# Optimization experiments

Measured on AMD Instinct MI355X. Metric: run time of the kernel, lower is better.

## Reference

```python
import jax, jax.numpy as jnp
import numpy as np
from jax.scipy.special import logsumexp

TEMPERATURE = 0.05
HARD_NEG_WEIGHT = 1.0
MARGIN = 0.2
EXPLICIT_NEG_WEIGHT = 2.0
NEG_INF = -1e9


def setup_inputs() -> dict:
    key = jax.random.key(0)
    k1, k2, k3 = jax.random.split(key, 3)
    N, D = 8192, 512
    return {
        "asm_embeddings": jax.random.normal(k1, (N, D), dtype=jnp.float32),
        "source_embeddings": jax.random.normal(k2, (N, D), dtype=jnp.float32),
        "labels": jax.random.randint(k3, (N,), 0, 2, dtype=jnp.int64),
    }


def reference(asm_embeddings, source_embeddings, labels):
    # L2-normalize both embedding sets
    a = asm_embeddings / jnp.linalg.norm(asm_embeddings, axis=1, keepdims=True)
    s = source_embeddings / jnp.linalg.norm(source_embeddings, axis=1, keepdims=True)
    sim = jnp.matmul(a, s.T) / TEMPERATURE  # [N, N]

    N = labels.shape[0]
    pos_mask = labels == 1
    neg_mask = labels == 0
    num_pos = jnp.sum(pos_mask).astype(sim.dtype)
    num_neg = jnp.sum(neg_mask)

    # column weights: explicit negatives (label==0) get EXPLICIT_NEG_WEIGHT,
    # others 1; the positive (diagonal) logit always has weight 1.
    log_w = jnp.log(jnp.where(neg_mask, EXPLICIT_NEG_WEIGHT, 1.0).astype(sim.dtype))
    eye = jnp.eye(N, dtype=bool)
    weighted_logits = sim + jnp.where(eye, 0.0, log_w[None, :])  # [N, N]

    lse = logsumexp(weighted_logits, axis=1)  # weighted logsumexp per row
    diag = jnp.diagonal(sim)
    per_row_loss = lse - diag  # -log_prob_pos

    infonce = jnp.sum(jnp.where(pos_mask, per_row_loss, 0.0)) / num_pos

    # margin penalty on hardest explicit-negative diagonal similarity
    mean_pos_sim = jnp.sum(jnp.where(pos_mask, diag, 0.0)) / num_pos
    hard_neg_sim = jnp.max(jnp.where(neg_mask, diag, NEG_INF))
    penalty = jax.nn.relu(hard_neg_sim - mean_pos_sim + MARGIN)
    penalty = jnp.where(num_neg > 0, penalty, 0.0)

    return infonce + HARD_NEG_WEIGHT * penalty
```

## Files before the change

kernel.cpp:

```cpp
#include <hip/hip_runtime.h>
#include <math.h>

#define NROWS 8192
#define DIM 512
#define INV_T 20.0f
#define QS 500.0f
#define DEQ2 (INV_T * 1.4426950408889634f / (QS * QS))

typedef __attribute__((ext_vector_type(4))) int i32x4;

__device__ __forceinline__ void gload_lds16(const void* g, void* l) {
    __builtin_amdgcn_global_load_lds(
        (const __attribute__((address_space(1))) unsigned int*)g,
        (__attribute__((address_space(3))) unsigned int*)l, 16, 0, 0);
}

__device__ __forceinline__ float hw_exp2(float x) {
    float r;
    asm("v_exp_f32 %0, %1" : "=v"(r) : "v"(x));
    return r;
}

__device__ __forceinline__ float dot4(float4 a, float4 b) {
    return a.x * b.x + a.y * b.y + a.z * b.z + a.w * b.w;
}

__device__ __forceinline__ int q4(float4 v, float s) {
    int b0 = __float2int_rn(fminf(fmaxf(v.x * s, -127.f), 127.f)) & 255;
    int b1 = __float2int_rn(fminf(fmaxf(v.y * s, -127.f), 127.f)) & 255;
    int b2 = __float2int_rn(fminf(fmaxf(v.z * s, -127.f), 127.f)) & 255;
    int b3 = __float2int_rn(fminf(fmaxf(v.w * s, -127.f), 127.f)) & 255;
    return b0 | (b1 << 8) | (b2 << 16) | (b3 << 24);
}

__global__ __launch_bounds__(256) void norm_kernel(
    const float* __restrict__ A, const float* __restrict__ S,
    const int* __restrict__ labels, signed char* __restrict__ aQ,
    signed char* __restrict__ sQ, float* __restrict__ diag,
    float* __restrict__ lw2, float* __restrict__ lsum) {
    const int wave = threadIdx.x >> 6, lane = threadIdx.x & 63;
    const int row = blockIdx.x * 4 + wave;
    const float4* a4 = (const float4*)(A + (size_t)row * DIM);
    const float4* s4 = (const float4*)(S + (size_t)row * DIM);
    float4 a0 = a4[lane], a1 = a4[lane + 64];
    float4 s0 = s4[lane], s1 = s4[lane + 64];
    float saa = dot4(a0, a0) + dot4(a1, a1);
    float sss = dot4(s0, s0) + dot4(s1, s1);
    float sas = dot4(a0, s0) + dot4(a1, s1);
    for (int m = 1; m < 64; m <<= 1) {
        saa += __shfl_xor(saa, m);
        sss += __shfl_xor(sss, m);
        sas += __shfl_xor(sas, m);
    }
    const float ra = rsqrtf(saa), rs = rsqrtf(sss);
    signed char* arow = aQ + (size_t)row * DIM;
    signed char* srow = sQ + (size_t)row * DIM;
    *(int*)(arow + lane * 4)       = q4(a0, ra * QS);
    *(int*)(arow + 256 + lane * 4) = q4(a1, ra * QS);
    *(int*)(srow + lane * 4)       = q4(s0, rs * QS);
    *(int*)(srow + 256 + lane * 4) = q4(s1, rs * QS);
    if (lane == 0) {
        diag[row] = sas * ra * rs * INV_T;
        lw2[row] = (labels[row] == 0) ? 1.0f : 0.0f;
        lsum[row] = 0.0f;
    }
}

__global__ __launch_bounds__(1024) void lse_gemm(
    const signed char* __restrict__ Aq, const signed char* __restrict__ Bq,
    const float* __restrict__ lw2, float* __restrict__ lsum) {
    __shared__ __align__(16) char lds[65536];

    const int bid = blockIdx.x;
    const int xcd = bid & 7, idx = bid >> 3;
    const int rt = (xcd >> 1) * 8 + (idx & 7);
    const int ctg = (xcd & 1) * 4 + (idx >> 3);
    const int row0 = rt * 256;
    const int colg = ctg * 1024;

    const int tid = threadIdx.x;
    const int wid = tid >> 6, lane = tid & 63;
    const int wr = wid >> 2, wc = wid & 3;
    const int fr = lane & 15, grp = lane >> 4;

    const int srow = tid >> 2;
    const int sl = (tid & 3) ^ ((tid >> 3) & 3);
    const signed char* aSrc = Aq + (size_t)(row0 + srow) * DIM + sl * 16;
    const signed char* bSrc = Bq + (size_t)(colg + srow) * DIM + sl * 16;
    char* dstA = lds + tid * 16;
    char* dstB = lds + 16384 + tid * 16;

#define STAGE(buf, TT)                                                        \
    do {                                                                      \
        const int ct_ = (TT) >> 3, k_ = (TT) & 7;                             \
        gload_lds16(aSrc + k_ * 64, dstA + (buf) * 32768);                    \
        gload_lds16(bSrc + ct_ * 131072 + k_ * 64, dstB + (buf) * 32768);     \
    } while (0)

    const int ps = (grp ^ ((fr >> 1) & 3)) << 4;
    const char* rdA = lds + (wr * 64 + fr) * 64 + ps;
    const char* rdB = lds + 16384 + (wc * 64 + fr) * 64 + ps;

    STAGE(0, 0);

    i32x4 acc[4][4] = {};
#pragma unroll 2
    for (int T = 0; T < 32; ++T) {
        const int buf = T & 1;
        if (T < 31) {
            STAGE(buf ^ 1, T + 1);
            asm volatile("s_waitcnt vmcnt(2)" ::: "memory");
        } else {
            asm volatile("s_waitcnt vmcnt(0)" ::: "memory");
        }
        __builtin_amdgcn_s_barrier();

        i32x4 a[4], b[4];
#pragma unroll
        for (int m = 0; m < 4; ++m)
            a[m] = *(const i32x4*)(rdA + buf * 32768 + m * 1024);
#pragma unroll
        for (int n = 0; n < 4; ++n)
            b[n] = *(const i32x4*)(rdB + buf * 32768 + n * 1024);
        asm volatile("s_waitcnt lgkmcnt(0)" ::: "memory");
        __builtin_amdgcn_sched_barrier(0);

        __builtin_amdgcn_s_setprio(1);
#pragma unroll
        for (int m = 0; m < 4; ++m)
#pragma unroll
            for (int n = 0; n < 4; ++n)
                acc[m][n] = __builtin_amdgcn_mfma_i32_16x16x64_i8(
                    a[m], b[n], acc[m][n], 0, 0, 0);
        __builtin_amdgcn_s_setprio(0);

        if ((T & 7) == 7) {
            const int ct = T >> 3;
            const int col0 = colg + ct * 256 + wc * 64;
            float lwv[4];
#pragma unroll
            for (int n = 0; n < 4; ++n)
                lwv[n] = lw2[col0 + n * 16 + fr];
#pragma unroll
            for (int m = 0; m < 4; ++m)
#pragma unroll
                for (int j = 0; j < 4; ++j) {
                    float s = 0.f;
#pragma unroll
                    for (int n = 0; n < 4; ++n)
                        s += hw_exp2(fmaf((float)acc[m][n][j], DEQ2, lwv[n]));
                    s += __shfl_xor(s, 1);
                    s += __shfl_xor(s, 2);
                    s += __shfl_xor(s, 4);
                    s += __shfl_xor(s, 8);
                    if (fr == 0)
                        atomicAdd(&lsum[row0 + wr * 64 + m * 16 + grp * 4 + j], s);
                }
#pragma unroll
            for (int m = 0; m < 4; ++m)
#pragma unroll
                for (int n = 0; n < 4; ++n)
                    acc[m][n] = i32x4{0, 0, 0, 0};
        }
        __builtin_amdgcn_s_barrier();
    }
#undef STAGE
}

__global__ __launch_bounds__(1024) void finalize_kernel(
    const float* __restrict__ lsum, const float* __restrict__ diag,
    const int* __restrict__ labels, float* __restrict__ out) {
    const int tid = threadIdx.x;
    float sl = 0.f, sd = 0.f, mx = -1e9f;
    int np_ = 0, nn_ = 0;
#pragma unroll
    for (int i = tid; i < NROWS; i += 1024) {
        const float dg = diag[i];
        if (labels[i] == 1) {
            sl += logf(lsum[i]) - dg;
            sd += dg;
            np_++;
        } else {
            nn_++;
            mx = fmaxf(mx, dg);
        }
    }
    for (int m = 1; m < 64; m <<= 1) {
        sl += __shfl_xor(sl, m);
        sd += __shfl_xor(sd, m);
        mx = fmaxf(mx, __shfl_xor(mx, m));
        np_ += __shfl_xor(np_, m);
        nn_ += __shfl_xor(nn_, m);
    }
    __shared__ float rsl[16], rsd[16], rmx[16];
    __shared__ int rnp[16], rnn[16];
    const int wave = tid >> 6, lane = tid & 63;
    if (lane == 0) {
        rsl[wave] = sl; rsd[wave] = sd; rmx[wave] = mx;
        rnp[wave] = np_; rnn[wave] = nn_;
    }
    __syncthreads();
    if (tid == 0) {
        float SL = 0.f, SD = 0.f, MX = -1e9f;
        int NP = 0, NN = 0;
        for (int w = 0; w < 16; w++) {
            SL += rsl[w]; SD += rsd[w]; MX = fmaxf(MX, rmx[w]);
            NP += rnp[w]; NN += rnn[w];
        }
        const float infonce = SL / (float)NP;
        const float meanpos = SD / (float)NP;
        float pen = fmaxf(MX - meanpos + 0.2f, 0.0f);
        if (NN == 0) pen = 0.0f;
        out[0] = infonce + pen;
    }
}

extern "C" void kernel_launch(void* const* d_in, const int* in_sizes, int n_in,
                              void* d_out, int out_size, void* d_ws, size_t ws_size,
                              hipStream_t stream) {
    const float* A = (const float*)d_in[0];
    const float* S = (const float*)d_in[1];
    const int* labels = (const int*)d_in[2];
    float* out = (float*)d_out;

    char* ws = (char*)d_ws;
    signed char* aQ = (signed char*)ws;
    signed char* sQ = (signed char*)(ws + (size_t)NROWS * DIM);
    char* p = ws + (size_t)NROWS * DIM * 2;
    float* diag = (float*)p;
    float* lw2 = (float*)(p + 32768);
    float* lsum = (float*)(p + 65536);

    norm_kernel<<<NROWS / 4, 256, 0, stream>>>(A, S, labels, aQ, sQ, diag, lw2, lsum);
    lse_gemm<<<256, 1024, 0, stream>>>(aQ, sQ, lw2, lsum);
    finalize_kernel<<<1, 1024, 0, stream>>>(lsum, diag, labels, out);
}
```

Baseline: 65.77 us.

## Retile LSE GEMM to 512-thread blocks with register-accumulated row sums

The int8 similarity GEMM now uses 512-thread blocks with 8 waves in a 4x2 layout. Each block covers 256 rows by 512 columns, processed as four 128-column tiles, and 512 blocks are launched. LDS per block drops to 48KB, which should allow more resident blocks per CU. Row exp-sums are now kept in registers across the column tiles, with one shuffle-and-atomic reduction at the end instead of one per tile. In exchange, each wave now loads A twice per stage and the total A-tile traffic doubles, and B tiles are reused across fewer rows per column.

```diff
diff --git a/kernel.cpp b/kernel.cpp
--- a/kernel.cpp
+++ b/kernel.cpp
@@ -66,35 +66,35 @@
     }
 }
 
-__global__ __launch_bounds__(1024) void lse_gemm(
+__global__ __launch_bounds__(512, 4) void lse_gemm(
     const signed char* __restrict__ Aq, const signed char* __restrict__ Bq,
     const float* __restrict__ lw2, float* __restrict__ lsum) {
-    __shared__ __align__(16) char lds[65536];
+    __shared__ __align__(16) char lds[49152];
 
     const int bid = blockIdx.x;
     const int xcd = bid & 7, idx = bid >> 3;
     const int rt = (xcd >> 1) * 8 + (idx & 7);
-    const int ctg = (xcd & 1) * 4 + (idx >> 3);
+    const int ctg = (xcd & 1) * 8 + (idx >> 3);
     const int row0 = rt * 256;
-    const int colg = ctg * 1024;
+    const int colg = ctg * 512;
 
     const int tid = threadIdx.x;
     const int wid = tid >> 6, lane = tid & 63;
-    const int wr = wid >> 2, wc = wid & 3;
+    const int wr = wid >> 1, wc = wid & 1;
     const int fr = lane & 15, grp = lane >> 4;
 
-    const int srow = tid >> 2;
     const int sl = (tid & 3) ^ ((tid >> 3) & 3);
-    const signed char* aSrc = Aq + (size_t)(row0 + srow) * DIM + sl * 16;
-    const signed char* bSrc = Bq + (size_t)(colg + srow) * DIM + sl * 16;
+    const signed char* aSrc = Aq + (size_t)(row0 + (tid >> 2)) * DIM + sl * 16;
+    const signed char* bSrc = Bq + (size_t)(colg + (tid >> 2)) * DIM + sl * 16;
     char* dstA = lds + tid * 16;
     char* dstB = lds + 16384 + tid * 16;
 
 #define STAGE(buf, TT)                                                        \
     do {                                                                      \
         const int ct_ = (TT) >> 3, k_ = (TT) & 7;                             \
-        gload_lds16(aSrc + k_ * 64, dstA + (buf) * 32768);                    \
-        gload_lds16(bSrc + ct_ * 131072 + k_ * 64, dstB + (buf) * 32768);     \
+        gload_lds16(aSrc + k_ * 64,           dstA + (buf) * 24576);          \
+        gload_lds16(aSrc + 65536 + k_ * 64,   dstA + (buf) * 24576 + 8192);   \
+        gload_lds16(bSrc + ct_ * 65536 + k_ * 64, dstB + (buf) * 24576);      \
     } while (0)
 
     const int ps = (grp ^ ((fr >> 1) & 3)) << 4;
@@ -103,68 +103,78 @@
 
     STAGE(0, 0);
 
+    float rsum[4][4] = {};
     i32x4 acc[4][4] = {};
-#pragma unroll 2
-    for (int T = 0; T < 32; ++T) {
-        const int buf = T & 1;
-        if (T < 31) {
-            STAGE(buf ^ 1, T + 1);
-            asm volatile("s_waitcnt vmcnt(2)" ::: "memory");
-        } else {
-            asm volatile("s_waitcnt vmcnt(0)" ::: "memory");
-        }
-        __builtin_amdgcn_s_barrier();
-
-        i32x4 a[4], b[4];
+
+#pragma unroll
+    for (int ct = 0; ct < 4; ++ct) {
+#pragma unroll
+        for (int k = 0; k < 8; ++k) {
+            const int T = ct * 8 + k;
+            const int buf = T & 1;
+            if (T < 31) {
+                STAGE(buf ^ 1, T + 1);
+                asm volatile("s_waitcnt vmcnt(3)" ::: "memory");
+            } else {
+                asm volatile("s_waitcnt vmcnt(0)" ::: "memory");
+            }
+            __builtin_amdgcn_s_barrier();
+
+            i32x4 a[4], b[4];
+#pragma unroll
+            for (int m = 0; m < 4; ++m)
+                a[m] = *(const i32x4*)(rdA + buf * 24576 + m * 1024);
+#pragma unroll
+            for (int n = 0; n < 4; ++n)
+                b[n] = *(const i32x4*)(rdB + buf * 24576 + n * 1024);
+            asm volatile("s_waitcnt lgkmcnt(0)" ::: "memory");
+            __builtin_amdgcn_sched_barrier(0);
+
+            __builtin_amdgcn_s_setprio(1);
+#pragma unroll
+            for (int m = 0; m < 4; ++m)
+#pragma unroll
+                for (int n = 0; n < 4; ++n)
+                    acc[m][n] = __builtin_amdgcn_mfma_i32_16x16x64_i8(
+                        a[m], b[n], acc[m][n], 0, 0, 0);
+            __builtin_amdgcn_s_setprio(0);
+            __builtin_amdgcn_s_barrier();
+        }
+
+        const int col0 = colg + ct * 128 + wc * 64;
+        float lwv[4];
+#pragma unroll
+        for (int n = 0; n < 4; ++n)
+            lwv[n] = lw2[col0 + n * 16 + fr];
 #pragma unroll
         for (int m = 0; m < 4; ++m)
-            a[m] = *(const i32x4*)(rdA + buf * 32768 + m * 1024);
-#pragma unroll
-        for (int n = 0; n < 4; ++n)
-            b[n] = *(const i32x4*)(rdB + buf * 32768 + n * 1024);
-        asm volatile("s_waitcnt lgkmcnt(0)" ::: "memory");
-        __builtin_amdgcn_sched_barrier(0);
-
-        __builtin_amdgcn_s_setprio(1);
+#pragma unroll
+            for (int j = 0; j < 4; ++j) {
+#pragma unroll
+                for (int n = 0; n < 4; ++n)
+                    rsum[m][j] +=
+                        hw_exp2(fmaf((float)acc[m][n][j], DEQ2, lwv[n]));
+            }
 #pragma unroll
         for (int m = 0; m < 4; ++m)
 #pragma unroll
             for (int n = 0; n < 4; ++n)
-                acc[m][n] = __builtin_amdgcn_mfma_i32_16x16x64_i8(
-                    a[m], b[n], acc[m][n], 0, 0, 0);
-        __builtin_amdgcn_s_setprio(0);
-
-        if ((T & 7) == 7) {
-            const int ct = T >> 3;
-            const int col0 = colg + ct * 256 + wc * 64;
-            float lwv[4];
-#pragma unroll
-            for (int n = 0; n < 4; ++n)
-                lwv[n] = lw2[col0 + n * 16 + fr];
-#pragma unroll
-            for (int m = 0; m < 4; ++m)
-#pragma unroll
-                for (int j = 0; j < 4; ++j) {
-                    float s = 0.f;
-#pragma unroll
-                    for (int n = 0; n < 4; ++n)
-                        s += hw_exp2(fmaf((float)acc[m][n][j], DEQ2, lwv[n]));
-                    s += __shfl_xor(s, 1);
-                    s += __shfl_xor(s, 2);
-                    s += __shfl_xor(s, 4);
-                    s += __shfl_xor(s, 8);
-                    if (fr == 0)
-                        atomicAdd(&lsum[row0 + wr * 64 + m * 16 + grp * 4 + j], s);
-                }
-#pragma unroll
-            for (int m = 0; m < 4; ++m)
-#pragma unroll
-                for (int n = 0; n < 4; ++n)
-                    acc[m][n] = i32x4{0, 0, 0, 0};
-        }
-        __builtin_amdgcn_s_barrier();
+                acc[m][n] = i32x4{0, 0, 0, 0};
     }
 #undef STAGE
+
+#pragma unroll
+    for (int m = 0; m < 4; ++m)
+#pragma unroll
+        for (int j = 0; j < 4; ++j) {
+            float v = rsum[m][j];
+            v += __shfl_xor(v, 1);
+            v += __shfl_xor(v, 2);
+            v += __shfl_xor(v, 4);
+            v += __shfl_xor(v, 8);
+            if (fr == 0)
+                atomicAdd(&lsum[row0 + wr * 64 + m * 16 + grp * 4 + j], v);
+        }
 }
 
 __global__ __launch_bounds__(1024) void finalize_kernel(
@@ -232,6 +242,6 @@
     float* lsum = (float*)(p + 65536);
 
     norm_kernel<<<NROWS / 4, 256, 0, stream>>>(A, S, labels, aQ, sQ, diag, lw2, lsum);
-    lse_gemm<<<256, 1024, 0, stream>>>(aQ, sQ, lw2, lsum);
+    lse_gemm<<<512, 512, 0, stream>>>(aQ, sQ, lw2, lsum);
     finalize_kernel<<<1, 1024, 0, stream>>>(lsum, diag, labels, out);
 }
```

Measured after the change: 163.6 us. 2.49x slower.

## Keep full-K A fragments in registers and stream B tiles per column block

Applied to the files above, without the earlier changes.

Restructures the int8 GEMM so each 512-thread block owns a 512x512 tile. Each wave first loads its whole 64-row A strip across all of K into registers, then streams 64-column B tiles of full K depth through double-buffered LDS, running the exp-sum epilogue after each column tile. This removes repeated A staging through LDS and halves the block size so two blocks can share a CU. In exchange the A fragments take a large register footprint, and each B tile carries a full vmcnt(0) wait plus barrier, which limits overlap of loads with compute.

```diff
diff --git a/kernel.cpp b/kernel.cpp
--- a/kernel.cpp
+++ b/kernel.cpp
@@ -66,105 +66,114 @@
     }
 }
 
-__global__ __launch_bounds__(1024) void lse_gemm(
+__global__ __launch_bounds__(512, 2) void lse_gemm(
     const signed char* __restrict__ Aq, const signed char* __restrict__ Bq,
     const float* __restrict__ lw2, float* __restrict__ lsum) {
     __shared__ __align__(16) char lds[65536];
 
     const int bid = blockIdx.x;
     const int xcd = bid & 7, idx = bid >> 3;
-    const int rt = (xcd >> 1) * 8 + (idx & 7);
-    const int ctg = (xcd & 1) * 4 + (idx >> 3);
-    const int row0 = rt * 256;
-    const int colg = ctg * 1024;
+    const int rt = (xcd >> 1) * 4 + (idx & 3);
+    const int cg = (xcd & 1) * 8 + (idx >> 2);
+    const int row0 = rt * 512;
+    const int colg = cg * 512;
 
     const int tid = threadIdx.x;
     const int wid = tid >> 6, lane = tid & 63;
-    const int wr = wid >> 2, wc = wid & 3;
     const int fr = lane & 15, grp = lane >> 4;
 
-    const int srow = tid >> 2;
-    const int sl = (tid & 3) ^ ((tid >> 3) & 3);
-    const signed char* aSrc = Aq + (size_t)(row0 + srow) * DIM + sl * 16;
-    const signed char* bSrc = Bq + (size_t)(colg + srow) * DIM + sl * 16;
-    char* dstA = lds + tid * 16;
-    char* dstB = lds + 16384 + tid * 16;
-
-#define STAGE(buf, TT)                                                        \
+    const int slA = (tid & 3) ^ ((tid >> 3) & 3);
+    const signed char* aSrc = Aq + (size_t)(row0 + (tid >> 2)) * DIM + slA * 16;
+#define STAGE_A(B, K)                                                         \
     do {                                                                      \
-        const int ct_ = (TT) >> 3, k_ = (TT) & 7;                             \
-        gload_lds16(aSrc + k_ * 64, dstA + (buf) * 32768);                    \
-        gload_lds16(bSrc + ct_ * 131072 + k_ * 64, dstB + (buf) * 32768);     \
+        _Pragma("unroll")                                                     \
+        for (int i = 0; i < 4; ++i)                                           \
+            gload_lds16(aSrc + (size_t)i * 65536 + (K) * 64,                  \
+                        lds + (B) * 32768 + i * 8192 + tid * 16);             \
     } while (0)
 
-    const int ps = (grp ^ ((fr >> 1) & 3)) << 4;
-    const char* rdA = lds + (wr * 64 + fr) * 64 + ps;
-    const char* rdB = lds + 16384 + (wc * 64 + fr) * 64 + ps;
-
-    STAGE(0, 0);
-
-    i32x4 acc[4][4] = {};
-#pragma unroll 2
-    for (int T = 0; T < 32; ++T) {
-        const int buf = T & 1;
-        if (T < 31) {
-            STAGE(buf ^ 1, T + 1);
-            asm volatile("s_waitcnt vmcnt(2)" ::: "memory");
-        } else {
-            asm volatile("s_waitcnt vmcnt(0)" ::: "memory");
+    const int slB = (tid & 31) ^ ((tid >> 5) & 7);
+    const signed char* bSrc = Bq + (size_t)(colg + (tid >> 5)) * DIM + slB * 16;
+#define STAGE_B(B, CT)                                                        \
+    do {                                                                      \
+        _Pragma("unroll")                                                     \
+        for (int i = 0; i < 4; ++i)                                           \
+            gload_lds16(bSrc + (size_t)(CT) * 32768 + i * 8192,               \
+                        lds + (B) * 32768 + i * 8192 + tid * 16);             \
+    } while (0)
+
+    const int psA = (grp ^ ((fr >> 1) & 3)) << 4;
+    const char* rdA = lds + (wid * 64 + fr) * 64 + psA;
+
+    i32x4 a[4][8];
+
+    STAGE_A(0, 0);
+    STAGE_A(1, 1);
+#pragma unroll
+    for (int k = 0; k < 8; ++k) {
+        if (k < 7)
+            asm volatile("s_waitcnt vmcnt(4)" ::: "memory");
+        else
+            asm volatile("s_waitcnt vmcnt(4)" ::: "memory");
+        __builtin_amdgcn_s_barrier();
+#pragma unroll
+        for (int m = 0; m < 4; ++m)
+            a[m][k] = *(const i32x4*)(rdA + (k & 1) * 32768 + m * 1024);
+        asm volatile("s_waitcnt lgkmcnt(0)" ::: "memory");
+        __builtin_amdgcn_s_barrier();
+        if (k < 6) STAGE_A(k & 1, k + 2);
+        if (k == 6) STAGE_B(0, 0);
+    }
+    asm volatile("s_waitcnt vmcnt(0)" ::: "memory");
+    __builtin_amdgcn_s_barrier();
+
+#pragma unroll 1
+    for (int ct = 0; ct < 8; ++ct) {
+        if (ct < 7) STAGE_B((ct + 1) & 1, ct + 1);
+
+        const char* rdB = lds + (ct & 1) * 32768;
+        i32x4 acc[4][4] = {};
+#pragma unroll
+        for (int k = 0; k < 8; ++k) {
+            i32x4 b[4];
+#pragma unroll
+            for (int n = 0; n < 4; ++n)
+                b[n] = *(const i32x4*)(rdB + (n * 16 + fr) * 512 +
+                                       (((k * 4 + grp) ^ (fr & 7)) << 4));
+#pragma unroll
+            for (int m = 0; m < 4; ++m)
+#pragma unroll
+                for (int n = 0; n < 4; ++n)
+                    acc[m][n] = __builtin_amdgcn_mfma_i32_16x16x64_i8(
+                        a[m][k], b[n], acc[m][n], 0, 0, 0);
         }
+
+        const int col0 = colg + ct * 64;
+        float lwv[4];
+#pragma unroll
+        for (int n = 0; n < 4; ++n)
+            lwv[n] = lw2[col0 + n * 16 + fr];
+#pragma unroll
+        for (int m = 0; m < 4; ++m)
+#pragma unroll
+            for (int j = 0; j < 4; ++j) {
+                float s = 0.f;
+#pragma unroll
+                for (int n = 0; n < 4; ++n)
+                    s += hw_exp2(fmaf((float)acc[m][n][j], DEQ2, lwv[n]));
+                s += __shfl_xor(s, 1);
+                s += __shfl_xor(s, 2);
+                s += __shfl_xor(s, 4);
+                s += __shfl_xor(s, 8);
+                if (fr == 0)
+                    atomicAdd(&lsum[row0 + wid * 64 + m * 16 + grp * 4 + j], s);
+            }
+
+        asm volatile("s_waitcnt vmcnt(0)" ::: "memory");
         __builtin_amdgcn_s_barrier();
-
-        i32x4 a[4], b[4];
-#pragma unroll
-        for (int m = 0; m < 4; ++m)
-            a[m] = *(const i32x4*)(rdA + buf * 32768 + m * 1024);
-#pragma unroll
-        for (int n = 0; n < 4; ++n)
-            b[n] = *(const i32x4*)(rdB + buf * 32768 + n * 1024);
-        asm volatile("s_waitcnt lgkmcnt(0)" ::: "memory");
-        __builtin_amdgcn_sched_barrier(0);
-
-        __builtin_amdgcn_s_setprio(1);
-#pragma unroll
-        for (int m = 0; m < 4; ++m)
-#pragma unroll
-            for (int n = 0; n < 4; ++n)
-                acc[m][n] = __builtin_amdgcn_mfma_i32_16x16x64_i8(
-                    a[m], b[n], acc[m][n], 0, 0, 0);
-        __builtin_amdgcn_s_setprio(0);
-
-        if ((T & 7) == 7) {
-            const int ct = T >> 3;
-            const int col0 = colg + ct * 256 + wc * 64;
-            float lwv[4];
-#pragma unroll
-            for (int n = 0; n < 4; ++n)
-                lwv[n] = lw2[col0 + n * 16 + fr];
-#pragma unroll
-            for (int m = 0; m < 4; ++m)
-#pragma unroll
-                for (int j = 0; j < 4; ++j) {
-                    float s = 0.f;
-#pragma unroll
-                    for (int n = 0; n < 4; ++n)
-                        s += hw_exp2(fmaf((float)acc[m][n][j], DEQ2, lwv[n]));
-                    s += __shfl_xor(s, 1);
-                    s += __shfl_xor(s, 2);
-                    s += __shfl_xor(s, 4);
-                    s += __shfl_xor(s, 8);
-                    if (fr == 0)
-                        atomicAdd(&lsum[row0 + wr * 64 + m * 16 + grp * 4 + j], s);
-                }
-#pragma unroll
-            for (int m = 0; m < 4; ++m)
-#pragma unroll
-                for (int n = 0; n < 4; ++n)
-                    acc[m][n] = i32x4{0, 0, 0, 0};
-        }
-        __builtin_amdgcn_s_barrier();
-    }
-#undef STAGE
+    }
+#undef STAGE_A
+#undef STAGE_B
 }
 
 __global__ __launch_bounds__(1024) void finalize_kernel(
@@ -232,6 +241,6 @@
     float* lsum = (float*)(p + 65536);
 
     norm_kernel<<<NROWS / 4, 256, 0, stream>>>(A, S, labels, aQ, sQ, diag, lw2, lsum);
-    lse_gemm<<<256, 1024, 0, stream>>>(aQ, sQ, lw2, lsum);
+    lse_gemm<<<256, 512, 0, stream>>>(aQ, sQ, lw2, lsum);
     finalize_kernel<<<1, 1024, 0, stream>>>(lsum, diag, labels, out);
 }
```

Measured after the change: 72.29 us. +9.9%, slower.

## Restructure int8 LSE GEMM into 512-thread triple-buffered phased pipeline

Applied to the files above, without the earlier changes.

Halves the workgroup to 8 waves, each computing a 128x64 output tile with 32 accumulators, so each B fragment loaded from LDS is reused twice as often. Staging moves from double to triple buffering in 96KB of LDS. Each K-step is split into four phases that interleave LDS fragment reads, one global-to-LDS prefetch each, and MFMA groups, with barriers between phases. It also remaps block IDs to XCDs differently. The aim is to hide load latency behind MFMA work and cut LDS traffic per MFMA, at the cost of higher register pressure, more barriers per step, and an occupancy hint of 2 blocks per CU that the LDS size probably cannot meet.

```diff
diff --git a/kernel.cpp b/kernel.cpp
--- a/kernel.cpp
+++ b/kernel.cpp
@@ -13,6 +13,12 @@
     __builtin_amdgcn_global_load_lds(
         (const __attribute__((address_space(1))) unsigned int*)g,
         (__attribute__((address_space(3))) unsigned int*)l, 16, 0, 0);
+}
+
+__device__ __forceinline__ void block_bar() {
+    asm volatile("" ::: "memory");
+    __builtin_amdgcn_s_barrier();
+    asm volatile("" ::: "memory");
 }
 
 __device__ __forceinline__ float hw_exp2(float x) {
@@ -66,15 +72,15 @@
     }
 }
 
-__global__ __launch_bounds__(1024) void lse_gemm(
+__global__ __launch_bounds__(512, 2) void lse_gemm(
     const signed char* __restrict__ Aq, const signed char* __restrict__ Bq,
     const float* __restrict__ lw2, float* __restrict__ lsum) {
-    __shared__ __align__(16) char lds[65536];
+    __shared__ __align__(16) char lds[98304];
 
     const int bid = blockIdx.x;
     const int xcd = bid & 7, idx = bid >> 3;
-    const int rt = (xcd >> 1) * 8 + (idx & 7);
-    const int ctg = (xcd & 1) * 4 + (idx >> 3);
+    const int rt = (xcd & 3) * 8 + (idx & 7);
+    const int ctg = (xcd >> 2) * 4 + (idx >> 3);
     const int row0 = rt * 256;
     const int colg = ctg * 1024;
 
@@ -83,56 +89,109 @@
     const int wr = wid >> 2, wc = wid & 3;
     const int fr = lane & 15, grp = lane >> 4;
 
-    const int srow = tid >> 2;
     const int sl = (tid & 3) ^ ((tid >> 3) & 3);
-    const signed char* aSrc = Aq + (size_t)(row0 + srow) * DIM + sl * 16;
-    const signed char* bSrc = Bq + (size_t)(colg + srow) * DIM + sl * 16;
-    char* dstA = lds + tid * 16;
-    char* dstB = lds + 16384 + tid * 16;
-
-#define STAGE(buf, TT)                                                        \
+    const signed char* aS = Aq + (size_t)(row0 + (tid >> 2)) * DIM + sl * 16;
+    const signed char* bS = Bq + (size_t)(colg + (tid >> 2)) * DIM + sl * 16;
+    char* dst = lds + tid * 16;
+
+#define STG(buf, TT, r)                                                       \
     do {                                                                      \
-        const int ct_ = (TT) >> 3, k_ = (TT) & 7;                             \
-        gload_lds16(aSrc + k_ * 64, dstA + (buf) * 32768);                    \
-        gload_lds16(bSrc + ct_ * 131072 + k_ * 64, dstB + (buf) * 32768);     \
+        if ((r) < 2)                                                          \
+            gload_lds16(aS + (r) * 65536 + ((TT) & 7) * 64,                   \
+                        dst + (buf) * 32768 + (r) * 8192);                    \
+        else                                                                  \
+            gload_lds16(bS + ((TT) >> 3) * 131072 + ((r) - 2) * 65536 +       \
+                            ((TT) & 7) * 64,                                  \
+                        dst + (buf) * 32768 + 16384 + ((r) - 2) * 8192);      \
     } while (0)
 
     const int ps = (grp ^ ((fr >> 1) & 3)) << 4;
-    const char* rdA = lds + (wr * 64 + fr) * 64 + ps;
+    const char* rdA = lds + (wr * 128 + fr) * 64 + ps;
     const char* rdB = lds + 16384 + (wc * 64 + fr) * 64 + ps;
 
-    STAGE(0, 0);
-
-    i32x4 acc[4][4] = {};
-#pragma unroll 2
+    STG(0, 0, 0); STG(0, 0, 1); STG(0, 0, 2); STG(0, 0, 3);
+    STG(1, 1, 0); STG(1, 1, 1); STG(1, 1, 2); STG(1, 1, 3);
+    asm volatile("s_waitcnt vmcnt(4)" ::: "memory");
+    block_bar();
+
+    i32x4 aLo[4], aHi[4], b[4];
+    i32x4 acc[8][4] = {};
+
+#pragma unroll 1
     for (int T = 0; T < 32; ++T) {
-        const int buf = T & 1;
-        if (T < 31) {
-            STAGE(buf ^ 1, T + 1);
-            asm volatile("s_waitcnt vmcnt(2)" ::: "memory");
-        } else {
-            asm volatile("s_waitcnt vmcnt(0)" ::: "memory");
-        }
-        __builtin_amdgcn_s_barrier();
-
-        i32x4 a[4], b[4];
-#pragma unroll
-        for (int m = 0; m < 4; ++m)
-            a[m] = *(const i32x4*)(rdA + buf * 32768 + m * 1024);
-#pragma unroll
-        for (int n = 0; n < 4; ++n)
+        const int buf = T % 3;
+        const int bufS = (T + 2) % 3;
+        const int pf = (T + 2 < 32);
+
+#pragma unroll
+        for (int m = 0; m < 4; ++m)
+            aLo[m] = *(const i32x4*)(rdA + buf * 32768 + m * 1024);
+#pragma unroll
+        for (int n = 0; n < 2; ++n)
             b[n] = *(const i32x4*)(rdB + buf * 32768 + n * 1024);
+        if (pf) STG(bufS, T + 2, 0);
+        block_bar();
         asm volatile("s_waitcnt lgkmcnt(0)" ::: "memory");
         __builtin_amdgcn_sched_barrier(0);
-
-        __builtin_amdgcn_s_setprio(1);
-#pragma unroll
-        for (int m = 0; m < 4; ++m)
-#pragma unroll
-            for (int n = 0; n < 4; ++n)
+        __builtin_amdgcn_s_setprio(1);
+#pragma unroll
+        for (int m = 0; m < 4; ++m)
+#pragma unroll
+            for (int n = 0; n < 2; ++n)
                 acc[m][n] = __builtin_amdgcn_mfma_i32_16x16x64_i8(
-                    a[m], b[n], acc[m][n], 0, 0, 0);
-        __builtin_amdgcn_s_setprio(0);
+                    aLo[m], b[n], acc[m][n], 0, 0, 0);
+        __builtin_amdgcn_s_setprio(0);
+        block_bar();
+
+#pragma unroll
+        for (int n = 2; n < 4; ++n)
+            b[n] = *(const i32x4*)(rdB + buf * 32768 + n * 1024);
+        if (pf) STG(bufS, T + 2, 1);
+        block_bar();
+        asm volatile("s_waitcnt lgkmcnt(0)" ::: "memory");
+        __builtin_amdgcn_sched_barrier(0);
+        __builtin_amdgcn_s_setprio(1);
+#pragma unroll
+        for (int m = 0; m < 4; ++m)
+#pragma unroll
+            for (int n = 2; n < 4; ++n)
+                acc[m][n] = __builtin_amdgcn_mfma_i32_16x16x64_i8(
+                    aLo[m], b[n], acc[m][n], 0, 0, 0);
+        __builtin_amdgcn_s_setprio(0);
+        block_bar();
+
+#pragma unroll
+        for (int m = 0; m < 4; ++m)
+            aHi[m] = *(const i32x4*)(rdA + buf * 32768 + 4096 + m * 1024);
+        if (pf) STG(bufS, T + 2, 2);
+        block_bar();
+        asm volatile("s_waitcnt lgkmcnt(0)" ::: "memory");
+        __builtin_amdgcn_sched_barrier(0);
+        __builtin_amdgcn_s_setprio(1);
+#pragma unroll
+        for (int m = 0; m < 4; ++m)
+#pragma unroll
+            for (int n = 2; n < 4; ++n)
+                acc[m + 4][n] = __builtin_amdgcn_mfma_i32_16x16x64_i8(
+                    aHi[m], b[n], acc[m + 4][n], 0, 0, 0);
+        __builtin_amdgcn_s_setprio(0);
+        block_bar();
+
+        if (pf) STG(bufS, T + 2, 3);
+        if (T <= 29)
+            asm volatile("s_waitcnt vmcnt(4)" ::: "memory");
+        else
+            asm volatile("s_waitcnt vmcnt(0)" ::: "memory");
+        block_bar();
+        __builtin_amdgcn_s_setprio(1);
+#pragma unroll
+        for (int m = 0; m < 4; ++m)
+#pragma unroll
+            for (int n = 0; n < 2; ++n)
+                acc[m + 4][n] = __builtin_amdgcn_mfma_i32_16x16x64_i8(
+                    aHi[m], b[n], acc[m + 4][n], 0, 0, 0);
+        __builtin_amdgcn_s_setprio(0);
+        block_bar();
 
         if ((T & 7) == 7) {
             const int ct = T >> 3;
@@ -142,7 +201,7 @@
             for (int n = 0; n < 4; ++n)
                 lwv[n] = lw2[col0 + n * 16 + fr];
 #pragma unroll
-            for (int m = 0; m < 4; ++m)
+            for (int m = 0; m < 8; ++m)
 #pragma unroll
                 for (int j = 0; j < 4; ++j) {
                     float s = 0.f;
@@ -154,17 +213,16 @@
                     s += __shfl_xor(s, 4);
                     s += __shfl_xor(s, 8);
                     if (fr == 0)
-                        atomicAdd(&lsum[row0 + wr * 64 + m * 16 + grp * 4 + j], s);
+                        atomicAdd(&lsum[row0 + wr * 128 + m * 16 + grp * 4 + j], s);
                 }
 #pragma unroll
-            for (int m = 0; m < 4; ++m)
+            for (int m = 0; m < 8; ++m)
 #pragma unroll
                 for (int n = 0; n < 4; ++n)
                     acc[m][n] = i32x4{0, 0, 0, 0};
         }
-        __builtin_amdgcn_s_barrier();
-    }
-#undef STAGE
+    }
+#undef STG
 }
 
 __global__ __launch_bounds__(1024) void finalize_kernel(
@@ -232,6 +290,6 @@
     float* lsum = (float*)(p + 65536);
 
     norm_kernel<<<NROWS / 4, 256, 0, stream>>>(A, S, labels, aQ, sQ, diag, lw2, lsum);
-    lse_gemm<<<256, 1024, 0, stream>>>(aQ, sQ, lw2, lsum);
+    lse_gemm<<<256, 512, 0, stream>>>(aQ, sQ, lw2, lsum);
     finalize_kernel<<<1, 1024, 0, stream>>>(lsum, diag, labels, out);
 }
```

Measured after the change: 77.77 us. 1.18x slower.
